# Performance work log

Hardware: AMD Instinct MI355X
Metric: run time of the kernel (lower is better)

## Reference

```python
import jax, jax.numpy as jnp
import numpy as np

B, DIM, HEADS, BLOCKS = 16, 192, 6, 6
H = W = 64
WS, SHIFT, MLP = 8, 4, 4
N = WS * WS
HD = DIM // HEADS
NW = (H // WS) * (W // WS)
SCALE = HD ** -0.5


def _ln(x, g, b, eps=1e-5):
    mu = jnp.mean(x, -1, keepdims=True)
    var = jnp.mean(jnp.square(x - mu), -1, keepdims=True)
    return (x - mu) * jax.lax.rsqrt(var + eps) * g + b


def _win_part(x):  # [B,H,W,C] -> [B*NW, N, C]
    x = x.reshape(B, H // WS, WS, W // WS, WS, DIM)
    return x.transpose(0, 1, 3, 2, 4, 5).reshape(-1, N, DIM)


def _win_rev(w):  # [B*NW, N, C] -> [B,H,W,C]
    x = w.reshape(B, H // WS, W // WS, WS, WS, DIM)
    return x.transpose(0, 1, 3, 2, 4, 5).reshape(B, H, W, DIM)


def _rel_pos_index():
    coords = np.stack(np.meshgrid(np.arange(WS), np.arange(WS), indexing='ij')).reshape(2, -1)
    rel = (coords[:, :, None] - coords[:, None, :]).transpose(1, 2, 0)
    rel[:, :, 0] += WS - 1
    rel[:, :, 1] += WS - 1
    rel[:, :, 0] *= 2 * WS - 1
    return jnp.asarray(rel.sum(-1))  # [N, N] int


def _attn_mask():  # shifted-window attention mask, [NW, N, N]
    img = np.zeros((H, W))
    cnt = 0
    for hs in (slice(0, -WS), slice(-WS, -SHIFT), slice(-SHIFT, None)):
        for ws_ in (slice(0, -WS), slice(-WS, -SHIFT), slice(-SHIFT, None)):
            img[hs, ws_] = cnt
            cnt += 1
    mw = img.reshape(H // WS, WS, W // WS, WS).transpose(0, 2, 1, 3).reshape(-1, N)
    am = mw[:, None, :] - mw[:, :, None]
    return jnp.asarray(np.where(am != 0, -100.0, 0.0).astype(np.float32))


RPI = _rel_pos_index()
MASK = _attn_mask()


def _block(x, shifted, n1g, n1b, qkvw, qkvb, pw, pb, rpb, n2g, n2b, f1w, f1b, f2w, f2b):
    shortcut = x  # [B, H*W, DIM]
    x = _ln(x, n1g, n1b).reshape(B, H, W, DIM)
    if shifted:
        x = jnp.roll(x, (-SHIFT, -SHIFT), (1, 2))
    xw = _win_part(x)  # [B*NW, N, DIM]
    qkv = (xw @ qkvw.T + qkvb).reshape(-1, N, 3, HEADS, HD).transpose(2, 0, 3, 1, 4)
    q, k, v = qkv[0], qkv[1], qkv[2]  # [B*NW, HEADS, N, HD]
    attn = jnp.einsum('bhnd,bhmd->bhnm', q * SCALE, k)
    attn = attn + rpb[RPI].transpose(2, 0, 1)[None]  # relative position bias
    if shifted:
        attn = (attn.reshape(B, NW, HEADS, N, N) + MASK[None, :, None]).reshape(-1, HEADS, N, N)
    attn = jax.nn.softmax(attn, -1)
    xw = jnp.einsum('bhnm,bhmd->bnhd', attn, v).reshape(-1, N, DIM)
    xw = xw @ pw.T + pb
    x = _win_rev(xw)
    if shifted:
        x = jnp.roll(x, (SHIFT, SHIFT), (1, 2))
    x = shortcut + x.reshape(B, H * W, DIM)
    h = _ln(x, n2g, n2b)
    h = jax.nn.gelu(h @ f1w.T + f1b, approximate=False) @ f2w.T + f2b
    return x + h


def _forward(x, en_g, en_b, n1_g, n1_b, qkv_w, qkv_b, proj_w, proj_b, rpb, n2_g, n2_b, fc1_w, fc1_b, fc2_w, fc2_b, fn_g, fn_b, conv_w):
    y = x.reshape(B, DIM, H * W).transpose(0, 2, 1)  # patch embed (patch_size=1)
    y = _ln(y, en_g, en_b)
    for i in range(BLOCKS):
        y = _block(y, i % 2 == 1, n1_g[i], n1_b[i], qkv_w[i], qkv_b[i], proj_w[i], proj_b[i],
                   rpb[i], n2_g[i], n2_b[i], fc1_w[i], fc1_b[i], fc2_w[i], fc2_b[i])
    y = _ln(y, fn_g, fn_b)
    y = y.transpose(0, 2, 1).reshape(B, DIM, H, W)  # patch unembed
    return y + jax.lax.conv_general_dilated(y, conv_w, (1, 1), 'SAME',
                                            dimension_numbers=('NCHW', 'OIHW', 'NCHW'))


def setup_inputs() -> dict:
    key = jax.random.key(0)
    ks = jax.random.split(key, 7)
    s = 0.02
    f32 = jnp.float32
    return {
        'x': jax.random.normal(ks[0], (B, DIM, H, W), f32),
        'en_g': jnp.ones((DIM,), f32), 'en_b': jnp.zeros((DIM,), f32),
        'n1_g': jnp.ones((BLOCKS, DIM), f32), 'n1_b': jnp.zeros((BLOCKS, DIM), f32),
        'qkv_w': s * jax.random.normal(ks[1], (BLOCKS, 3 * DIM, DIM), f32),
        'qkv_b': jnp.zeros((BLOCKS, 3 * DIM), f32),
        'proj_w': s * jax.random.normal(ks[2], (BLOCKS, DIM, DIM), f32),
        'proj_b': jnp.zeros((BLOCKS, DIM), f32),
        'rpb': s * jax.random.normal(ks[3], (BLOCKS, (2 * WS - 1) ** 2, HEADS), f32),
        'n2_g': jnp.ones((BLOCKS, DIM), f32), 'n2_b': jnp.zeros((BLOCKS, DIM), f32),
        'fc1_w': s * jax.random.normal(ks[4], (BLOCKS, MLP * DIM, DIM), f32),
        'fc1_b': jnp.zeros((BLOCKS, MLP * DIM), f32),
        'fc2_w': s * jax.random.normal(ks[5], (BLOCKS, DIM, MLP * DIM), f32),
        'fc2_b': jnp.zeros((BLOCKS, DIM), f32),
        'fn_g': jnp.ones((DIM,), f32), 'fn_b': jnp.zeros((DIM,), f32),
        'conv_w': s * jax.random.normal(ks[6], (DIM, DIM, 3, 3), f32),
    }


def reference(x, en_g, en_b, n1_g, n1_b, qkv_w, qkv_b, proj_w, proj_b, rpb, n2_g, n2_b, fc1_w, fc1_b, fc2_w, fc2_b, fn_g, fn_b, conv_w):
    return _forward(x, en_g, en_b, n1_g, n1_b, qkv_w, qkv_b, proj_w, proj_b, rpb,
                    n2_g, n2_b, fc1_w, fc1_b, fc2_w, fc2_b, fn_g, fn_b, conv_w)
```

## Files before the change

kernel.cpp:

```cpp
#include <hip/hip_runtime.h>
#include <cstdint>
#include <cstddef>

#define BATCH 16
#define DIM 192
#define HEADS 6
#define HD 32
#define TOK 65536
#define QKV_D 576
#define MLP_D 768
#define SCALE 0.17677669529663687f

#define CH 32768

typedef __bf16 bf16x8 __attribute__((ext_vector_type(8)));
typedef float f32x4 __attribute__((ext_vector_type(4)));

__device__ __forceinline__ unsigned short f2bf(float f) {
  union { float f; unsigned u; } c;
  c.f = f;
  return (unsigned short)((c.u + 0x7fffu + ((c.u >> 16) & 1)) >> 16);
}

__device__ __forceinline__ float waveSum(float v) {
#pragma unroll
  for (int off = 32; off; off >>= 1) v += __shfl_xor(v, off, 64);
  return v;
}

__device__ __forceinline__ float rowSum16(float v) {
  v += __shfl_xor(v, 1, 64);
  v += __shfl_xor(v, 2, 64);
  v += __shfl_xor(v, 4, 64);
  v += __shfl_xor(v, 8, 64);
  return v;
}

#define GLD(SRC, DST)                                                     \
  __builtin_amdgcn_global_load_lds(                                       \
      (const __attribute__((address_space(1))) void*)(SRC),               \
      (__attribute__((address_space(3))) void*)(DST), 16, 0, 0)

__global__ __launch_bounds__(64) void zero_k(float* p) { p[threadIdx.x] = 0.f; }

__global__ __launch_bounds__(256) void cvt_k(const float* __restrict__ s,
                                             unsigned short* __restrict__ d,
                                             int n) {
  int i = ((blockIdx.x << 8) + threadIdx.x) << 2;
  if (i < n) {
    float4 v = *(const float4*)(s + i);
    d[i] = f2bf(v.x);
    d[i + 1] = f2bf(v.y);
    d[i + 2] = f2bf(v.z);
    d[i + 3] = f2bf(v.w);
  }
}

__global__ __launch_bounds__(256) void cvt_qkv_k(const float* __restrict__ s,
                                                 unsigned short* __restrict__ d) {
  int i = (blockIdx.x << 8) + threadIdx.x;
  if (i < 663552) {
    int r = (i / 192) % 576;
    float v = s[i];
    if (r < 192) v *= SCALE;
    d[i] = f2bf(v);
  }
}

__global__ __launch_bounds__(256) void scale_qkvb_k(const float* __restrict__ s,
                                                    float* __restrict__ d) {
  int i = (blockIdx.x << 8) + threadIdx.x;
  if (i < 3456) {
    float v = s[i];
    if ((i % 576) < 192) v *= SCALE;
    d[i] = v;
  }
}

__global__ __launch_bounds__(256) void cvt_conv_k(const float* __restrict__ s,
                                                  unsigned short* __restrict__ d) {
  int i = (blockIdx.x << 8) + threadIdx.x;
  if (i < 331776) {
    int o = i / 1728;
    int r = i - o * 1728;
    int tap = r / 192;
    int ci = r - tap * 192;
    d[i] = f2bf(s[o * 1728 + ci * 9 + tap]);
  }
}

__global__ __launch_bounds__(256) void embed_ln_t_k(
    const float* __restrict__ x, const float* __restrict__ g,
    const float* __restrict__ be, float* __restrict__ y) {
  __shared__ float ts[192 * 65];
  const int w = threadIdx.x >> 6, lane = threadIdx.x & 63;
  const int t0 = blockIdx.x << 6;
  const int b = t0 >> 12, tb = t0 & 4095;
  const float* xb = x + (((size_t)b * DIM) << 12) + tb;
#pragma unroll
  for (int j = 0; j < 48; ++j) {
    int ch = w * 48 + j;
    ts[ch * 65 + lane] = xb[((size_t)ch << 12) + lane];
  }
  __syncthreads();
#pragma unroll 4
  for (int idx = 0; idx < 16; ++idx) {
    int tk = (w << 4) + idx;
    float v0 = ts[lane * 65 + tk];
    float v1 = ts[(lane + 64) * 65 + tk];
    float v2 = ts[(lane + 128) * 65 + tk];
    float mu = waveSum(v0 + v1 + v2) * (1.f / 192.f);
    float d0 = v0 - mu, d1 = v1 - mu, d2 = v2 - mu;
    float var = waveSum(d0 * d0 + d1 * d1 + d2 * d2) * (1.f / 192.f);
    float rs = rsqrtf(var + 1e-5f);
    float* yp = y + (size_t)(t0 + tk) * DIM;
    yp[lane] = d0 * rs * g[lane] + be[lane];
    yp[lane + 64] = d1 * rs * g[lane + 64] + be[lane + 64];
    yp[lane + 128] = d2 * rs * g[lane + 128] + be[lane + 128];
  }
}

__global__ __launch_bounds__(256) void ln_final_k(
    float* __restrict__ y, const float* __restrict__ g,
    const float* __restrict__ be, unsigned short* __restrict__ hb) {
  int tok = (blockIdx.x << 2) + (threadIdx.x >> 6);
  int lane = threadIdx.x & 63;
  float* yp = y + (size_t)tok * DIM;
  float v0 = yp[lane], v1 = yp[lane + 64], v2 = yp[lane + 128];
  float mu = waveSum(v0 + v1 + v2) * (1.f / 192.f);
  float d0 = v0 - mu, d1 = v1 - mu, d2 = v2 - mu;
  float var = waveSum(d0 * d0 + d1 * d1 + d2 * d2) * (1.f / 192.f);
  float rs = rsqrtf(var + 1e-5f);
  float r0 = d0 * rs * g[lane] + be[lane];
  float r1 = d1 * rs * g[lane + 64] + be[lane + 64];
  float r2 = d2 * rs * g[lane + 128] + be[lane + 128];
  yp[lane] = r0;
  yp[lane + 64] = r1;
  yp[lane + 128] = r2;
  unsigned short* op = hb + (size_t)tok * DIM;
  op[lane] = f2bf(r0);
  op[lane + 64] = f2bf(r1);
  op[lane + 128] = f2bf(r2);
}

__global__ __launch_bounds__(256) void ln_window_k(
    const float* __restrict__ y, const float* __restrict__ g,
    const float* __restrict__ be, unsigned short* __restrict__ xw,
    int shifted) {
  int m = (blockIdx.x << 2) + (threadIdx.x >> 6);
  int lane = threadIdx.x & 63;
  int widx = m >> 6, n = m & 63;
  int b = widx >> 6, win = widx & 63;
  int hp = ((win >> 3) << 3) + (n >> 3);
  int wp = ((win & 7) << 3) + (n & 7);
  if (shifted) { hp = (hp + 4) & 63; wp = (wp + 4) & 63; }
  int src = (b << 12) + (hp << 6) + wp;
  const float* yp = y + (size_t)src * DIM;
  float v0 = yp[lane], v1 = yp[lane + 64], v2 = yp[lane + 128];
  float mu = waveSum(v0 + v1 + v2) * (1.f / 192.f);
  float d0 = v0 - mu, d1 = v1 - mu, d2 = v2 - mu;
  float var = waveSum(d0 * d0 + d1 * d1 + d2 * d2) * (1.f / 192.f);
  float rs = rsqrtf(var + 1e-5f);
  unsigned short* op = xw + (size_t)m * DIM;
  op[lane] = f2bf(d0 * rs * g[lane] + be[lane]);
  op[lane + 64] = f2bf(d1 * rs * g[lane + 64] + be[lane + 64]);
  op[lane + 128] = f2bf(d2 * rs * g[lane + 128] + be[lane + 128]);
}

__global__ __launch_bounds__(64) void attn_k(
    const unsigned short* __restrict__ qkv, const float* __restrict__ rpb,
    unsigned short* __restrict__ out, int shifted, int widx0) {
  __shared__ unsigned short vt[32 * 72];
  __shared__ unsigned short pl[64 * 72];
  __shared__ float rp[228];
  const int lwidx = blockIdx.x / HEADS;
  const int head = blockIdx.x - lwidx * HEADS;
  const int l = threadIdx.x;
  const int g = l >> 4, li = l & 15;

  for (int i = l; i < 225; i += 64) rp[i] = rpb[i * HEADS + head];

  const unsigned short* base = qkv + (size_t)lwidx * 64 * QKV_D + head * HD;

  bf16x8 qf[4], kf[4];
#pragma unroll
  for (int n = 0; n < 4; ++n)
    qf[n] = *(const bf16x8*)(base + (size_t)(16 * n + li) * QKV_D + g * 8);
#pragma unroll
  for (int i = 0; i < 4; ++i)
    kf[i] = *(const bf16x8*)(base + (size_t)(16 * i + li) * QKV_D + DIM + g * 8);

#pragma unroll
  for (int p = 0; p < 4; ++p) {
    int r = 16 * p + (l >> 2);
    int d0 = (l & 3) << 3;
    bf16x8 v8 = *(const bf16x8*)(base + (size_t)r * QKV_D + 2 * DIM + d0);
#pragma unroll
    for (int e = 0; e < 8; ++e)
      vt[(d0 + e) * 72 + r] = ((const unsigned short*)&v8)[e];
  }

  f32x4 s[4][4] = {};
#pragma unroll
  for (int i = 0; i < 4; ++i)
#pragma unroll
    for (int n = 0; n < 4; ++n)
      s[i][n] = __builtin_amdgcn_mfma_f32_16x16x32_bf16(kf[i], qf[n], s[i][n],
                                                        0, 0, 0);
  __syncthreads();

  const int win = (widx0 + lwidx) & 63;
  const int wh = (win >> 3) << 3, wwp = (win & 7) << 3;
  int rq[4], cq[4], zq[4];
#pragma unroll
  for (int n = 0; n < 4; ++n) {
    int q = 16 * n + li;
    rq[n] = q >> 3;
    cq[n] = q & 7;
    zq[n] = 0;
    if (shifted) {
      int hq = wh + rq[n], wq = wwp + cq[n];
      int zr = hq < 56 ? 0 : (hq < 60 ? 1 : 2);
      int zc = wq < 56 ? 0 : (wq < 60 ? 1 : 2);
      zq[n] = 3 * zr + zc;
    }
  }
#pragma unroll
  for (int i = 0; i < 4; ++i)
#pragma unroll
    for (int j = 0; j < 4; ++j) {
      int m = 16 * i + 4 * g + j;
      int rm = m >> 3, cm = m & 7;
      int zm = 0;
      if (shifted) {
        int hm = wh + rm, wm = wwp + cm;
        int zr = hm < 56 ? 0 : (hm < 60 ? 1 : 2);
        int zc = wm < 56 ? 0 : (wm < 60 ? 1 : 2);
        zm = 3 * zr + zc;
      }
#pragma unroll
      for (int n = 0; n < 4; ++n) {
        float b = rp[(rq[n] - rm + 7) * 15 + (cq[n] - cm + 7)];
        if (shifted && zm != zq[n]) b -= 100.f;
        s[i][n][j] += b;
      }
    }

  float inv[4];
#pragma unroll
  for (int n = 0; n < 4; ++n) {
    float m0 = -1e30f;
#pragma unroll
    for (int i = 0; i < 4; ++i)
#pragma unroll
      for (int j = 0; j < 4; ++j) m0 = fmaxf(m0, s[i][n][j]);
    m0 = fmaxf(m0, __shfl_xor(m0, 16, 64));
    m0 = fmaxf(m0, __shfl_xor(m0, 32, 64));
    float s0 = 0.f;
#pragma unroll
    for (int i = 0; i < 4; ++i)
#pragma unroll
      for (int j = 0; j < 4; ++j) {
        float e = __expf(s[i][n][j] - m0);
        s[i][n][j] = e;
        s0 += e;
      }
    s0 += __shfl_xor(s0, 16, 64);
    s0 += __shfl_xor(s0, 32, 64);
    inv[n] = 1.f / s0;
  }

#pragma unroll
  for (int n = 0; n < 4; ++n) {
    int q = 16 * n + li;
#pragma unroll
    for (int i = 0; i < 4; ++i) {
      unsigned lo = (unsigned)f2bf(s[i][n][0]) | ((unsigned)f2bf(s[i][n][1]) << 16);
      unsigned hi = (unsigned)f2bf(s[i][n][2]) | ((unsigned)f2bf(s[i][n][3]) << 16);
      *(uint2*)&pl[q * 72 + 16 * i + 4 * g] = uint2{lo, hi};
    }
  }
  __syncthreads();

  f32x4 o[2][4] = {};
#pragma unroll
  for (int ks = 0; ks < 2; ++ks) {
    bf16x8 va[2], pb[4];
#pragma unroll
    for (int i2 = 0; i2 < 2; ++i2)
      va[i2] = *(const bf16x8*)&vt[(16 * i2 + li) * 72 + 32 * ks + 8 * g];
#pragma unroll
    for (int n2 = 0; n2 < 4; ++n2)
      pb[n2] = *(const bf16x8*)&pl[(16 * n2 + li) * 72 + 32 * ks + 8 * g];
#pragma unroll
    for (int i2 = 0; i2 < 2; ++i2)
#pragma unroll
      for (int n2 = 0; n2 < 4; ++n2)
        o[i2][n2] = __builtin_amdgcn_mfma_f32_16x16x32_bf16(va[i2], pb[n2],
                                                            o[i2][n2], 0, 0, 0);
  }

  unsigned short* ob = out + (size_t)(lwidx * 64) * DIM + head * HD;
#pragma unroll
  for (int i2 = 0; i2 < 2; ++i2)
#pragma unroll
    for (int n2 = 0; n2 < 4; ++n2) {
      int q = 16 * n2 + li;
      float iv = inv[n2];
      unsigned lo = (unsigned)f2bf(o[i2][n2][0] * iv) |
                    ((unsigned)f2bf(o[i2][n2][1] * iv) << 16);
      unsigned hi = (unsigned)f2bf(o[i2][n2][2] * iv) |
                    ((unsigned)f2bf(o[i2][n2][3] * iv) << 16);
      *(uint2*)(ob + (size_t)q * DIM + 16 * i2 + 4 * g) = uint2{lo, hi};
    }
}

__device__ __forceinline__ void mfma_block256(const unsigned short* As,
                                              const unsigned short* Bs,
                                              f32x4 acc[4][4], int w,
                                              int lane) {
  const int frow = lane & 15;
  const int fk = (lane >> 4) << 3;
#pragma unroll
  for (int kk = 0; kk < 64; kk += 32) {
    int slotk = (kk + fk) >> 3;
    bf16x8 a[4], b[4];
#pragma unroll
    for (int m = 0; m < 4; ++m) {
      int ar = (w << 6) + (m << 4) + frow;
      a[m] = *(const bf16x8*)&As[(ar << 6) + ((slotk ^ (ar & 7)) << 3)];
    }
#pragma unroll
    for (int n = 0; n < 4; ++n) {
      int br = (n << 4) + frow;
      b[n] = *(const bf16x8*)&Bs[(br << 6) + ((slotk ^ (br & 7)) << 3)];
    }
#pragma unroll
    for (int m = 0; m < 4; ++m)
#pragma unroll
      for (int n = 0; n < 4; ++n)
        acc[m][n] =
            __builtin_amdgcn_mfma_f32_16x16x32_bf16(a[m], b[n], acc[m][n], 0,
                                                    0, 0);
  }
}

__device__ __forceinline__ void mfma_block128(const unsigned short* As,
                                              const unsigned short* Bs,
                                              f32x4 acc[2][4], int w,
                                              int lane) {
  const int frow = lane & 15;
  const int fk = (lane >> 4) << 3;
#pragma unroll
  for (int kk = 0; kk < 64; kk += 32) {
    int slotk = (kk + fk) >> 3;
    int ar0 = (w << 5) + frow, ar1 = ar0 + 16;
    bf16x8 a0 = *(const bf16x8*)&As[(ar0 << 6) + ((slotk ^ (ar0 & 7)) << 3)];
    bf16x8 a1 = *(const bf16x8*)&As[(ar1 << 6) + ((slotk ^ (ar1 & 7)) << 3)];
    bf16x8 b[4];
#pragma unroll
    for (int n = 0; n < 4; ++n) {
      int br = (n << 4) + frow;
      b[n] = *(const bf16x8*)&Bs[(br << 6) + ((slotk ^ (br & 7)) << 3)];
    }
#pragma unroll
    for (int n = 0; n < 4; ++n) {
      acc[0][n] = __builtin_amdgcn_mfma_f32_16x16x32_bf16(a0, b[n], acc[0][n], 0, 0, 0);
      acc[1][n] = __builtin_amdgcn_mfma_f32_16x16x32_bf16(a1, b[n], acc[1][n], 0, 0, 0);
    }
  }
}

template <int EPI>
__global__ __launch_bounds__(256) void mgemm_k(
    const unsigned short* __restrict__ A, const unsigned short* __restrict__ W,
    const float* __restrict__ bias, void* __restrict__ Cv, int N, int K) {
  __shared__ unsigned short As[256 * 64];
  __shared__ unsigned short Bs[64 * 64];
  const int tid = threadIdx.x;
  const int w = tid >> 6, lane = tid & 63;
  const int row0 = blockIdx.x << 8;
  const int col0 = blockIdx.y << 6;
  f32x4 acc[4][4] = {};

  for (int k0 = 0; k0 < K; k0 += 64) {
    if (k0) __syncthreads();
#pragma unroll
    for (int r = 0; r < 2; ++r) {
      int q = (r << 8) + tid;
      int brow = q >> 3, cs = q & 7;
      int kg = cs ^ (brow & 7);
      GLD(W + (size_t)(col0 + brow) * K + k0 + (kg << 3),
          Bs + (((r << 8) + (w << 6)) << 3));
    }
#pragma unroll
    for (int r = 0; r < 8; ++r) {
      int q = (r << 8) + tid;
      int arow = q >> 3, cs = q & 7;
      int kg = cs ^ (arow & 7);
      GLD(A + (size_t)(row0 + arow) * K + k0 + (kg << 3),
          As + (((r << 8) + (w << 6)) << 3));
    }
    __syncthreads();
    mfma_block256(As, Bs, acc, w, lane);
  }

  const int erow = (lane >> 4) << 2;
  const int ecol = lane & 15;
#pragma unroll
  for (int mr = 0; mr < 4; ++mr)
#pragma unroll
    for (int nr = 0; nr < 4; ++nr)
#pragma unroll
      for (int j = 0; j < 4; ++j) {
        int row = row0 + (w << 6) + (mr << 4) + erow + j;
        int col = col0 + (nr << 4) + ecol;
        float v = acc[mr][nr][j];
        ((unsigned short*)Cv)[(size_t)row * N + col] = f2bf(v + bias[col]);
      }
}

__global__ __launch_bounds__(256) void wgemm_k(
    const unsigned short* __restrict__ A, const unsigned short* __restrict__ W,
    const float* __restrict__ bias, float* __restrict__ y,
    unsigned short* __restrict__ lnout, const float* __restrict__ g,
    const float* __restrict__ be, int K, int sh2) {
  __shared__ unsigned short As[64 * 64];
  __shared__ unsigned short Bs[192 * 64];
  const int tid = threadIdx.x;
  const int w = tid >> 6, lane = tid & 63;
  const int row0 = blockIdx.x << 6;
  f32x4 acc[12] = {};

  for (int k0 = 0; k0 < K; k0 += 64) {
    if (k0) __syncthreads();
#pragma unroll
    for (int r = 0; r < 6; ++r) {
      int q = (r << 8) + tid;
      int brow = q >> 3, cs = q & 7;
      int kg = cs ^ (brow & 7);
      GLD(W + (size_t)brow * K + k0 + (kg << 3),
          Bs + (((r << 8) + (w << 6)) << 3));
    }
#pragma unroll
    for (int r = 0; r < 2; ++r) {
      int q = (r << 8) + tid;
      int arow = q >> 3, cs = q & 7;
      int kg = cs ^ (arow & 7);
      GLD(A + (size_t)(row0 + arow) * K + k0 + (kg << 3),
          As + (((r << 8) + (w << 6)) << 3));
    }
    __syncthreads();
    const int frow = lane & 15;
    const int fk = (lane >> 4) << 3;
#pragma unroll
    for (int kk = 0; kk < 64; kk += 32) {
      int slotk = (kk + fk) >> 3;
      int ar = (w << 4) + frow;
      bf16x8 a = *(const bf16x8*)&As[(ar << 6) + ((slotk ^ (ar & 7)) << 3)];
      bf16x8 b[12];
#pragma unroll
      for (int n = 0; n < 12; ++n) {
        int br = (n << 4) + frow;
        b[n] = *(const bf16x8*)&Bs[(br << 6) + ((slotk ^ (br & 7)) << 3)];
      }
#pragma unroll
      for (int n = 0; n < 12; ++n)
        acc[n] = __builtin_amdgcn_mfma_f32_16x16x32_bf16(a, b[n], acc[n], 0, 0,
                                                         0);
    }
  }

  const int erow = (lane >> 4) << 2;
  const int ecol = lane & 15;
  float bv[12], gv[12], bev[12];
#pragma unroll
  for (int n = 0; n < 12; ++n) {
    int col = (n << 4) + ecol;
    bv[n] = bias[col];
    gv[n] = g[col];
    bev[n] = be[col];
  }

#pragma unroll
  for (int j = 0; j < 4; ++j) {
    int m = row0 + (w << 4) + erow + j;
    int n64 = m & 63, widx = m >> 6;
    int bl = widx >> 6, win = widx & 63;
    int hp = ((win >> 3) << 3) + (n64 >> 3);
    int wp = ((win & 7) << 3) + (n64 & 7);
    if (sh2) { hp = (hp + 4) & 63; wp = (wp + 4) & 63; }
    int tok = (bl << 12) + (hp << 6) + wp;
    float* yp = y + (size_t)tok * DIM;
    float v[12];
    float s0 = 0.f;
#pragma unroll
    for (int n = 0; n < 12; ++n) {
      v[n] = acc[n][j] + bv[n] + yp[(n << 4) + ecol];
      s0 += v[n];
    }
#pragma unroll
    for (int n = 0; n < 12; ++n) yp[(n << 4) + ecol] = v[n];
    float mu = rowSum16(s0) * (1.f / 192.f);
    float s1 = 0.f;
#pragma unroll
    for (int n = 0; n < 12; ++n) {
      float d = v[n] - mu;
      s1 += d * d;
    }
    float rs = rsqrtf(rowSum16(s1) * (1.f / 192.f) + 1e-5f);
    unsigned short* op = lnout + (size_t)tok * DIM;
#pragma unroll
    for (int n = 0; n < 12; ++n)
      op[(n << 4) + ecol] = f2bf((v[n] - mu) * rs * gv[n] + bev[n]);
  }
}

template <int LAST>
__global__ __launch_bounds__(256) void mlp_k(
    const unsigned short* __restrict__ A, const unsigned short* __restrict__ W1,
    const float* __restrict__ b1, const unsigned short* __restrict__ W2,
    const float* __restrict__ b2, float* __restrict__ y,
    unsigned short* __restrict__ lnout, const float* __restrict__ g,
    const float* __restrict__ be, int sh2) {
  __shared__ unsigned short As[64 * 192];
  __shared__ unsigned short Bsw[192 * 64];
  __shared__ unsigned short hc[64 * 64];
  __shared__ float b1s[768];
  const int tid = threadIdx.x;
  const int w = tid >> 6, lane = tid & 63;
  const int row0 = blockIdx.x << 6;
  const int frow = lane & 15;
  const int fk = (lane >> 4) << 3;
  const int erow = (lane >> 4) << 2;
  const int ecol = lane & 15;

#pragma unroll
  for (int r = 0; r < 6; ++r) {
    int q = (r << 8) + tid;
    int kb = q >> 9, row = (q >> 3) & 63, cs = q & 7;
    int kg = cs ^ (row & 7);
    GLD(A + (size_t)(row0 + row) * 192 + kb * 64 + (kg << 3),
        As + (((r << 8) + (w << 6)) << 3));
  }
  for (int i = tid; i < 768; i += 256) b1s[i] = b1[i];

  f32x4 acc2[12] = {};

  for (int n0 = 0; n0 < 12; ++n0) {
    __syncthreads();
#pragma unroll
    for (int r = 0; r < 6; ++r) {
      int q = (r << 8) + tid;
      int kb = q >> 9, row = (q >> 3) & 63, cs = q & 7;
      int kg = cs ^ (row & 7);
      GLD(W1 + (size_t)(n0 * 64 + row) * 192 + kb * 64 + (kg << 3),
          Bsw + (((r << 8) + (w << 6)) << 3));
    }
    __syncthreads();
    f32x4 acc1[4] = {};
#pragma unroll
    for (int kk = 0; kk < 192; kk += 32) {
      int kb = kk >> 6;
      int slotk = ((kk & 63) + fk) >> 3;
      int ar = (w << 4) + frow;
      bf16x8 a = *(const bf16x8*)&As[(kb << 12) + (ar << 6) +
                                     ((slotk ^ (ar & 7)) << 3)];
#pragma unroll
      for (int n = 0; n < 4; ++n) {
        int br = (n << 4) + frow;
        bf16x8 b = *(const bf16x8*)&Bsw[(kb << 12) + (br << 6) +
                                        ((slotk ^ (br & 7)) << 3)];
        acc1[n] = __builtin_amdgcn_mfma_f32_16x16x32_bf16(a, b, acc1[n], 0, 0, 0);
      }
    }
#pragma unroll
    for (int n = 0; n < 4; ++n)
#pragma unroll
      for (int j = 0; j < 4; ++j) {
        int hr = (w << 4) + erow + j;
        int hcol = (n << 4) + ecol;
        float xg = acc1[n][j] + b1s[n0 * 64 + hcol];
        float hv = 0.5f * xg * (1.f + erff(xg * 0.7071067811865475f));
        hc[(hr << 6) + (((hcol >> 3) ^ (hr & 7)) << 3) + (hcol & 7)] = f2bf(hv);
      }
    __syncthreads();
#pragma unroll
    for (int r = 0; r < 6; ++r) {
      int q = (r << 8) + tid;
      int row = q >> 3, cs = q & 7;
      int kg = cs ^ (row & 7);
      GLD(W2 + (size_t)row * 768 + n0 * 64 + (kg << 3),
          Bsw + (((r << 8) + (w << 6)) << 3));
    }
    __syncthreads();
#pragma unroll
    for (int kk = 0; kk < 64; kk += 32) {
      int slotk = (kk + fk) >> 3;
      int ar = (w << 4) + frow;
      bf16x8 a = *(const bf16x8*)&hc[(ar << 6) + ((slotk ^ (ar & 7)) << 3)];
#pragma unroll
      for (int n = 0; n < 12; ++n) {
        int br = (n << 4) + frow;
        bf16x8 b = *(const bf16x8*)&Bsw[(br << 6) + ((slotk ^ (br & 7)) << 3)];
        acc2[n] = __builtin_amdgcn_mfma_f32_16x16x32_bf16(a, b, acc2[n], 0, 0, 0);
      }
    }
  }

  float bv[12], gv[12], bev[12];
#pragma unroll
  for (int n = 0; n < 12; ++n) {
    int col = (n << 4) + ecol;
    bv[n] = b2[col];
    if (LAST == 0) { gv[n] = g[col]; bev[n] = be[col]; }
  }

#pragma unroll
  for (int j = 0; j < 4; ++j) {
    int tok = row0 + (w << 4) + erow + j;
    float* yp = y + (size_t)tok * DIM;
    float v[12];
    float s0 = 0.f;
#pragma unroll
    for (int n = 0; n < 12; ++n) {
      v[n] = acc2[n][j] + bv[n] + yp[(n << 4) + ecol];
      s0 += v[n];
    }
#pragma unroll
    for (int n = 0; n < 12; ++n) yp[(n << 4) + ecol] = v[n];
    if (LAST == 0) {
      float mu = rowSum16(s0) * (1.f / 192.f);
      float s1 = 0.f;
#pragma unroll
      for (int n = 0; n < 12; ++n) {
        float d = v[n] - mu;
        s1 += d * d;
      }
      float rs = rsqrtf(rowSum16(s1) * (1.f / 192.f) + 1e-5f);
      int hw = tok & 4095;
      int gi = tok >> 12;
      int h = hw >> 6, ww = hw & 63;
      int hs = sh2 ? (h + 60) & 63 : h;
      int ws = sh2 ? (ww + 60) & 63 : ww;
      int win = ((hs >> 3) << 3) | (ws >> 3);
      int n64 = ((hs & 7) << 3) | (ws & 7);
      size_t drow = ((size_t)gi << 12) + (win << 6) + n64;
      unsigned short* op = lnout + drow * DIM;
#pragma unroll
      for (int n = 0; n < 12; ++n)
        op[(n << 4) + ecol] = f2bf((v[n] - mu) * rs * gv[n] + bev[n]);
    }
  }
}

__global__ __launch_bounds__(256) void conv_k(
    const unsigned short* __restrict__ A, const unsigned short* __restrict__ W,
    float* __restrict__ out, const float* __restrict__ Z,
    const unsigned short* __restrict__ zpg) {
  __shared__ unsigned short As[128 * 64];
  __shared__ unsigned short Bs[64 * 64];
  const int tid = threadIdx.x;
  const int w = tid >> 6, lane = tid & 63;
  const int row0 = blockIdx.x << 7;
  const int col0 = blockIdx.y << 6;
  f32x4 acc[2][4] = {};
  bool first = true;

#pragma unroll
  for (int tap = 0; tap < 9; ++tap) {
    const int dh = tap / 3 - 1, dw = tap % 3 - 1;
#pragma unroll
    for (int k0 = 0; k0 < 192; k0 += 64) {
      if (!first) __syncthreads();
      first = false;
#pragma unroll
      for (int r = 0; r < 2; ++r) {
        int q = (r << 8) + tid;
        int brow = q >> 3, cs = q & 7;
        int kg = cs ^ (brow & 7);
        GLD(W + (size_t)(col0 + brow) * 1728 + tap * 192 + k0 + (kg << 3),
            Bs + (((r << 8) + (w << 6)) << 3));
      }
#pragma unroll
      for (int r = 0; r < 4; ++r) {
        int q = (r << 8) + tid;
        int arow = q >> 3, cs = q & 7;
        int kg = cs ^ (arow & 7);
        int m = row0 + arow;
        int hw_ = m & 4095;
        int h = hw_ >> 6, ww = hw_ & 63;
        int ih = h + dh, iw = ww + dw;
        const unsigned short* src =
            ((unsigned)ih < 64u && (unsigned)iw < 64u)
                ? A + (size_t)(m + dh * 64 + dw) * DIM + k0 + (kg << 3)
                : zpg;
        GLD(src, As + (((r << 8) + (w << 6)) << 3));
      }
      __syncthreads();
      mfma_block128(As, Bs, acc, w, lane);
    }
  }

  const int erow = (lane >> 4) << 2;
  const int ecol = lane & 15;
#pragma unroll
  for (int mr = 0; mr < 2; ++mr)
#pragma unroll
    for (int nr = 0; nr < 4; ++nr)
#pragma unroll
      for (int j = 0; j < 4; ++j) {
        int row = row0 + (w << 5) + (mr << 4) + erow + j;
        int col = col0 + (nr << 4) + ecol;
        int b = row >> 12, hw_ = row & 4095;
        out[(((size_t)(b * DIM + col)) << 12) + hw_] =
            acc[mr][nr][j] + Z[(size_t)row * DIM + col];
      }
}

extern "C" void kernel_launch(void* const* d_in, const int* in_sizes, int n_in,
                              void* d_out, int out_size, void* d_ws,
                              size_t ws_size, hipStream_t stream) {
  const float* x = (const float*)d_in[0];
  const float* en_g = (const float*)d_in[1];
  const float* en_b = (const float*)d_in[2];
  const float* n1_g = (const float*)d_in[3];
  const float* n1_b = (const float*)d_in[4];
  const float* qkv_w = (const float*)d_in[5];
  const float* qkv_b = (const float*)d_in[6];
  const float* proj_w = (const float*)d_in[7];
  const float* proj_b = (const float*)d_in[8];
  const float* rpb = (const float*)d_in[9];
  const float* n2_g = (const float*)d_in[10];
  const float* n2_b = (const float*)d_in[11];
  const float* fc1_w = (const float*)d_in[12];
  const float* fc1_b = (const float*)d_in[13];
  const float* fc2_w = (const float*)d_in[14];
  const float* fc2_b = (const float*)d_in[15];
  const float* fn_g = (const float*)d_in[16];
  const float* fn_b = (const float*)d_in[17];
  const float* conv_w = (const float*)d_in[18];
  float* out = (float*)d_out;

  float* y = (float*)d_ws;
  unsigned short* buf1 = (unsigned short*)((char*)d_ws + 50331648);
  unsigned short* buf2u = (unsigned short*)((char*)d_ws + 75497472);
  unsigned short* ln2buf = buf2u;
  unsigned short* wbuf = (unsigned short*)((char*)d_ws + 113246208);
  unsigned short* zpg = (unsigned short*)((char*)d_ws + 119218176);
  float* qkv_bs = (float*)((char*)d_ws + 119218432);

  unsigned short* qkv_wb = wbuf;
  unsigned short* proj_wb = wbuf + 663552;
  unsigned short* fc1_wb = wbuf + 884736;
  unsigned short* fc2_wb = wbuf + 1769472;
  unsigned short* conv_wb = wbuf + 2654208;

  zero_k<<<1, 64, 0, stream>>>((float*)zpg);
  cvt_qkv_k<<<2592, 256, 0, stream>>>(qkv_w, qkv_wb);
  scale_qkvb_k<<<14, 256, 0, stream>>>(qkv_b, qkv_bs);
  cvt_k<<<216, 256, 0, stream>>>(proj_w, proj_wb, 221184);
  cvt_k<<<864, 256, 0, stream>>>(fc1_w, fc1_wb, 884736);
  cvt_k<<<864, 256, 0, stream>>>(fc2_w, fc2_wb, 884736);
  cvt_conv_k<<<1296, 256, 0, stream>>>(conv_w, conv_wb);

  embed_ln_t_k<<<1024, 256, 0, stream>>>(x, en_g, en_b, y);
  ln_window_k<<<16384, 256, 0, stream>>>(y, n1_g, n1_b, buf1, 0);

  for (int i = 0; i < 6; ++i) {
    int sh = i & 1;
    for (int c = 0; c < 2; ++c) {
      unsigned short* b1c = buf1 + (size_t)c * CH * DIM;
      mgemm_k<3><<<dim3(CH / 256, 9), 256, 0, stream>>>(
          b1c, qkv_wb + (size_t)i * QKV_D * DIM, qkv_bs + i * QKV_D, buf2u,
          QKV_D, DIM);
      attn_k<<<(CH / 64) * HEADS, 64, 0, stream>>>(
          buf2u, rpb + i * 225 * HEADS, b1c, sh, c * (CH / 64));
    }
    wgemm_k<<<TOK / 64, 256, 0, stream>>>(
        buf1, proj_wb + (size_t)i * DIM * DIM, proj_b + i * DIM, y, ln2buf,
        n2_g + i * DIM, n2_b + i * DIM, DIM, sh);
    if (i < 5) {
      mlp_k<0><<<TOK / 64, 256, 0, stream>>>(
          ln2buf, fc1_wb + (size_t)i * MLP_D * DIM, fc1_b + i * MLP_D,
          fc2_wb + (size_t)i * DIM * MLP_D, fc2_b + i * DIM, y, buf1,
          n1_g + (i + 1) * DIM, n1_b + (i + 1) * DIM, (i + 1) & 1);
    } else {
      mlp_k<1><<<TOK / 64, 256, 0, stream>>>(
          ln2buf, fc1_wb + (size_t)i * MLP_D * DIM, fc1_b + i * MLP_D,
          fc2_wb + (size_t)i * DIM * MLP_D, fc2_b + i * DIM, y, buf1, fn_g,
          fn_b, 0);
    }
  }

  ln_final_k<<<16384, 256, 0, stream>>>(y, fn_g, fn_b, buf1);
  conv_k<<<dim3(TOK / 128, 3), 256, 0, stream>>>(buf1, conv_wb, out, y, zpg);
}
```

Measured before the change: 1.386 ms.

## Double row tile in proj and MLP kernels, load A fragments directly from global

The projection GEMM and fused MLP kernels now process 128 rows per block (32 per wave, two MFMA row tiles) instead of 64, halving the number of blocks and the number of times weight tiles are staged into LDS. The A operand is no longer staged in shared memory. Each wave reads its bf16x8 fragments straight from global memory, which cuts LDS use and barriers but relies on cache hits for the repeated A reads. Accumulator registers double, which may lower occupancy, and the fc1 stage now reloads A from global on every one of the 12 n0 iterations.

```diff
diff --git a/kernel.cpp b/kernel.cpp
--- a/kernel.cpp
+++ b/kernel.cpp
@@ -425,12 +425,13 @@
     const float* __restrict__ bias, float* __restrict__ y,
     unsigned short* __restrict__ lnout, const float* __restrict__ g,
     const float* __restrict__ be, int K, int sh2) {
-  __shared__ unsigned short As[64 * 64];
   __shared__ unsigned short Bs[192 * 64];
   const int tid = threadIdx.x;
   const int w = tid >> 6, lane = tid & 63;
-  const int row0 = blockIdx.x << 6;
-  f32x4 acc[12] = {};
+  const int row0 = blockIdx.x << 7;
+  const int frow = lane & 15;
+  const int fk = (lane >> 4) << 3;
+  f32x4 acc[2][12] = {};
 
   for (int k0 = 0; k0 < K; k0 += 64) {
     if (k0) __syncthreads();
@@ -442,32 +443,23 @@
       GLD(W + (size_t)brow * K + k0 + (kg << 3),
           Bs + (((r << 8) + (w << 6)) << 3));
     }
-#pragma unroll
-    for (int r = 0; r < 2; ++r) {
-      int q = (r << 8) + tid;
-      int arow = q >> 3, cs = q & 7;
-      int kg = cs ^ (arow & 7);
-      GLD(A + (size_t)(row0 + arow) * K + k0 + (kg << 3),
-          As + (((r << 8) + (w << 6)) << 3));
-    }
     __syncthreads();
-    const int frow = lane & 15;
-    const int fk = (lane >> 4) << 3;
 #pragma unroll
     for (int kk = 0; kk < 64; kk += 32) {
       int slotk = (kk + fk) >> 3;
-      int ar = (w << 4) + frow;
-      bf16x8 a = *(const bf16x8*)&As[(ar << 6) + ((slotk ^ (ar & 7)) << 3)];
-      bf16x8 b[12];
-#pragma unroll
-      for (int n = 0; n < 12; ++n) {
-        int br = (n << 4) + frow;
-        b[n] = *(const bf16x8*)&Bs[(br << 6) + ((slotk ^ (br & 7)) << 3)];
-      }
-#pragma unroll
-      for (int n = 0; n < 12; ++n)
-        acc[n] = __builtin_amdgcn_mfma_f32_16x16x32_bf16(a, b[n], acc[n], 0, 0,
-                                                         0);
+#pragma unroll
+      for (int m = 0; m < 2; ++m) {
+        int ar = row0 + (w << 5) + (m << 4) + frow;
+        bf16x8 a = *(const bf16x8*)(A + (size_t)ar * K + k0 + kk + fk);
+        bf16x8 b;
+#pragma unroll
+        for (int n = 0; n < 12; ++n) {
+          int br = (n << 4) + frow;
+          b = *(const bf16x8*)&Bs[(br << 6) + ((slotk ^ (br & 7)) << 3)];
+          acc[m][n] = __builtin_amdgcn_mfma_f32_16x16x32_bf16(a, b, acc[m][n],
+                                                              0, 0, 0);
+        }
+      }
     }
   }
 
@@ -483,37 +475,39 @@
   }
 
 #pragma unroll
-  for (int j = 0; j < 4; ++j) {
-    int m = row0 + (w << 4) + erow + j;
-    int n64 = m & 63, widx = m >> 6;
-    int bl = widx >> 6, win = widx & 63;
-    int hp = ((win >> 3) << 3) + (n64 >> 3);
-    int wp = ((win & 7) << 3) + (n64 & 7);
-    if (sh2) { hp = (hp + 4) & 63; wp = (wp + 4) & 63; }
-    int tok = (bl << 12) + (hp << 6) + wp;
-    float* yp = y + (size_t)tok * DIM;
-    float v[12];
-    float s0 = 0.f;
-#pragma unroll
-    for (int n = 0; n < 12; ++n) {
-      v[n] = acc[n][j] + bv[n] + yp[(n << 4) + ecol];
-      s0 += v[n];
-    }
-#pragma unroll
-    for (int n = 0; n < 12; ++n) yp[(n << 4) + ecol] = v[n];
-    float mu = rowSum16(s0) * (1.f / 192.f);
-    float s1 = 0.f;
-#pragma unroll
-    for (int n = 0; n < 12; ++n) {
-      float d = v[n] - mu;
-      s1 += d * d;
-    }
-    float rs = rsqrtf(rowSum16(s1) * (1.f / 192.f) + 1e-5f);
-    unsigned short* op = lnout + (size_t)tok * DIM;
-#pragma unroll
-    for (int n = 0; n < 12; ++n)
-      op[(n << 4) + ecol] = f2bf((v[n] - mu) * rs * gv[n] + bev[n]);
-  }
+  for (int mr = 0; mr < 2; ++mr)
+#pragma unroll
+    for (int j = 0; j < 4; ++j) {
+      int m = row0 + (w << 5) + (mr << 4) + erow + j;
+      int n64 = m & 63, widx = m >> 6;
+      int bl = widx >> 6, win = widx & 63;
+      int hp = ((win >> 3) << 3) + (n64 >> 3);
+      int wp = ((win & 7) << 3) + (n64 & 7);
+      if (sh2) { hp = (hp + 4) & 63; wp = (wp + 4) & 63; }
+      int tok = (bl << 12) + (hp << 6) + wp;
+      float* yp = y + (size_t)tok * DIM;
+      float v[12];
+      float s0 = 0.f;
+#pragma unroll
+      for (int n = 0; n < 12; ++n) {
+        v[n] = acc[mr][n][j] + bv[n] + yp[(n << 4) + ecol];
+        s0 += v[n];
+      }
+#pragma unroll
+      for (int n = 0; n < 12; ++n) yp[(n << 4) + ecol] = v[n];
+      float mu = rowSum16(s0) * (1.f / 192.f);
+      float s1 = 0.f;
+#pragma unroll
+      for (int n = 0; n < 12; ++n) {
+        float d = v[n] - mu;
+        s1 += d * d;
+      }
+      float rs = rsqrtf(rowSum16(s1) * (1.f / 192.f) + 1e-5f);
+      unsigned short* op = lnout + (size_t)tok * DIM;
+#pragma unroll
+      for (int n = 0; n < 12; ++n)
+        op[(n << 4) + ecol] = f2bf((v[n] - mu) * rs * gv[n] + bev[n]);
+    }
 }
 
 template <int LAST>
@@ -523,29 +517,20 @@
     const float* __restrict__ b2, float* __restrict__ y,
     unsigned short* __restrict__ lnout, const float* __restrict__ g,
     const float* __restrict__ be, int sh2) {
-  __shared__ unsigned short As[64 * 192];
   __shared__ unsigned short Bsw[192 * 64];
-  __shared__ unsigned short hc[64 * 64];
+  __shared__ unsigned short hc[128 * 64];
   __shared__ float b1s[768];
   const int tid = threadIdx.x;
   const int w = tid >> 6, lane = tid & 63;
-  const int row0 = blockIdx.x << 6;
+  const int row0 = blockIdx.x << 7;
   const int frow = lane & 15;
   const int fk = (lane >> 4) << 3;
   const int erow = (lane >> 4) << 2;
   const int ecol = lane & 15;
 
-#pragma unroll
-  for (int r = 0; r < 6; ++r) {
-    int q = (r << 8) + tid;
-    int kb = q >> 9, row = (q >> 3) & 63, cs = q & 7;
-    int kg = cs ^ (row & 7);
-    GLD(A + (size_t)(row0 + row) * 192 + kb * 64 + (kg << 3),
-        As + (((r << 8) + (w << 6)) << 3));
-  }
   for (int i = tid; i < 768; i += 256) b1s[i] = b1[i];
 
-  f32x4 acc2[12] = {};
+  f32x4 acc2[2][12] = {};
 
   for (int n0 = 0; n0 < 12; ++n0) {
     __syncthreads();
@@ -558,32 +543,38 @@
           Bsw + (((r << 8) + (w << 6)) << 3));
     }
     __syncthreads();
-    f32x4 acc1[4] = {};
+    f32x4 acc1[2][4] = {};
 #pragma unroll
     for (int kk = 0; kk < 192; kk += 32) {
       int kb = kk >> 6;
       int slotk = ((kk & 63) + fk) >> 3;
-      int ar = (w << 4) + frow;
-      bf16x8 a = *(const bf16x8*)&As[(kb << 12) + (ar << 6) +
-                                     ((slotk ^ (ar & 7)) << 3)];
-#pragma unroll
-      for (int n = 0; n < 4; ++n) {
-        int br = (n << 4) + frow;
-        bf16x8 b = *(const bf16x8*)&Bsw[(kb << 12) + (br << 6) +
-                                        ((slotk ^ (br & 7)) << 3)];
-        acc1[n] = __builtin_amdgcn_mfma_f32_16x16x32_bf16(a, b, acc1[n], 0, 0, 0);
-      }
-    }
-#pragma unroll
-    for (int n = 0; n < 4; ++n)
-#pragma unroll
-      for (int j = 0; j < 4; ++j) {
-        int hr = (w << 4) + erow + j;
-        int hcol = (n << 4) + ecol;
-        float xg = acc1[n][j] + b1s[n0 * 64 + hcol];
-        float hv = 0.5f * xg * (1.f + erff(xg * 0.7071067811865475f));
-        hc[(hr << 6) + (((hcol >> 3) ^ (hr & 7)) << 3) + (hcol & 7)] = f2bf(hv);
-      }
+#pragma unroll
+      for (int m = 0; m < 2; ++m) {
+        int ar = row0 + (w << 5) + (m << 4) + frow;
+        bf16x8 a = *(const bf16x8*)(A + (size_t)ar * 192 + kk + fk);
+#pragma unroll
+        for (int n = 0; n < 4; ++n) {
+          int br = (n << 4) + frow;
+          bf16x8 b = *(const bf16x8*)&Bsw[(kb << 12) + (br << 6) +
+                                          ((slotk ^ (br & 7)) << 3)];
+          acc1[m][n] =
+              __builtin_amdgcn_mfma_f32_16x16x32_bf16(a, b, acc1[m][n], 0, 0, 0);
+        }
+      }
+    }
+#pragma unroll
+    for (int m = 0; m < 2; ++m)
+#pragma unroll
+      for (int n = 0; n < 4; ++n)
+#pragma unroll
+        for (int j = 0; j < 4; ++j) {
+          int hr = (w << 5) + (m << 4) + erow + j;
+          int hcol = (n << 4) + ecol;
+          float xg = acc1[m][n][j] + b1s[n0 * 64 + hcol];
+          float hv = 0.5f * xg * (1.f + erff(xg * 0.7071067811865475f));
+          hc[(hr << 6) + (((hcol >> 3) ^ (hr & 7)) << 3) + (hcol & 7)] =
+              f2bf(hv);
+        }
     __syncthreads();
 #pragma unroll
     for (int r = 0; r < 6; ++r) {
@@ -597,13 +588,18 @@
 #pragma unroll
     for (int kk = 0; kk < 64; kk += 32) {
       int slotk = (kk + fk) >> 3;
-      int ar = (w << 4) + frow;
-      bf16x8 a = *(const bf16x8*)&hc[(ar << 6) + ((slotk ^ (ar & 7)) << 3)];
-#pragma unroll
-      for (int n = 0; n < 12; ++n) {
-        int br = (n << 4) + frow;
-        bf16x8 b = *(const bf16x8*)&Bsw[(br << 6) + ((slotk ^ (br & 7)) << 3)];
-        acc2[n] = __builtin_amdgcn_mfma_f32_16x16x32_bf16(a, b, acc2[n], 0, 0, 0);
+#pragma unroll
+      for (int m = 0; m < 2; ++m) {
+        int ar = (w << 5) + (m << 4) + frow;
+        bf16x8 a = *(const bf16x8*)&hc[(ar << 6) + ((slotk ^ (ar & 7)) << 3)];
+#pragma unroll
+        for (int n = 0; n < 12; ++n) {
+          int br = (n << 4) + frow;
+          bf16x8 b =
+              *(const bf16x8*)&Bsw[(br << 6) + ((slotk ^ (br & 7)) << 3)];
+          acc2[m][n] =
+              __builtin_amdgcn_mfma_f32_16x16x32_bf16(a, b, acc2[m][n], 0, 0, 0);
+        }
       }
     }
   }
@@ -617,41 +613,43 @@
   }
 
 #pragma unroll
-  for (int j = 0; j < 4; ++j) {
-    int tok = row0 + (w << 4) + erow + j;
-    float* yp = y + (size_t)tok * DIM;
-    float v[12];
-    float s0 = 0.f;
-#pragma unroll
-    for (int n = 0; n < 12; ++n) {
-      v[n] = acc2[n][j] + bv[n] + yp[(n << 4) + ecol];
-      s0 += v[n];
-    }
-#pragma unroll
-    for (int n = 0; n < 12; ++n) yp[(n << 4) + ecol] = v[n];
-    if (LAST == 0) {
-      float mu = rowSum16(s0) * (1.f / 192.f);
-      float s1 = 0.f;
+  for (int mr = 0; mr < 2; ++mr)
+#pragma unroll
+    for (int j = 0; j < 4; ++j) {
+      int tok = row0 + (w << 5) + (mr << 4) + erow + j;
+      float* yp = y + (size_t)tok * DIM;
+      float v[12];
+      float s0 = 0.f;
 #pragma unroll
       for (int n = 0; n < 12; ++n) {
-        float d = v[n] - mu;
-        s1 += d * d;
-      }
-      float rs = rsqrtf(rowSum16(s1) * (1.f / 192.f) + 1e-5f);
-      int hw = tok & 4095;
-      int gi = tok >> 12;
-      int h = hw >> 6, ww = hw & 63;
-      int hs = sh2 ? (h + 60) & 63 : h;
-      int ws = sh2 ? (ww + 60) & 63 : ww;
-      int win = ((hs >> 3) << 3) | (ws >> 3);
-      int n64 = ((hs & 7) << 3) | (ws & 7);
-      size_t drow = ((size_t)gi << 12) + (win << 6) + n64;
-      unsigned short* op = lnout + drow * DIM;
-#pragma unroll
-      for (int n = 0; n < 12; ++n)
-        op[(n << 4) + ecol] = f2bf((v[n] - mu) * rs * gv[n] + bev[n]);
-    }
-  }
+        v[n] = acc2[mr][n][j] + bv[n] + yp[(n << 4) + ecol];
+        s0 += v[n];
+      }
+#pragma unroll
+      for (int n = 0; n < 12; ++n) yp[(n << 4) + ecol] = v[n];
+      if (LAST == 0) {
+        float mu = rowSum16(s0) * (1.f / 192.f);
+        float s1 = 0.f;
+#pragma unroll
+        for (int n = 0; n < 12; ++n) {
+          float d = v[n] - mu;
+          s1 += d * d;
+        }
+        float rs = rsqrtf(rowSum16(s1) * (1.f / 192.f) + 1e-5f);
+        int hw = tok & 4095;
+        int gi = tok >> 12;
+        int h = hw >> 6, ww = hw & 63;
+        int hs = sh2 ? (h + 60) & 63 : h;
+        int ws = sh2 ? (ww + 60) & 63 : ww;
+        int win = ((hs >> 3) << 3) | (ws >> 3);
+        int n64 = ((hs & 7) << 3) | (ws & 7);
+        size_t drow = ((size_t)gi << 12) + (win << 6) + n64;
+        unsigned short* op = lnout + drow * DIM;
+#pragma unroll
+        for (int n = 0; n < 12; ++n)
+          op[(n << 4) + ecol] = f2bf((v[n] - mu) * rs * gv[n] + bev[n]);
+      }
+    }
 }
 
 __global__ __launch_bounds__(256) void conv_k(
@@ -777,16 +775,16 @@
       attn_k<<<(CH / 64) * HEADS, 64, 0, stream>>>(
           buf2u, rpb + i * 225 * HEADS, b1c, sh, c * (CH / 64));
     }
-    wgemm_k<<<TOK / 64, 256, 0, stream>>>(
+    wgemm_k<<<TOK / 128, 256, 0, stream>>>(
         buf1, proj_wb + (size_t)i * DIM * DIM, proj_b + i * DIM, y, ln2buf,
         n2_g + i * DIM, n2_b + i * DIM, DIM, sh);
     if (i < 5) {
-      mlp_k<0><<<TOK / 64, 256, 0, stream>>>(
+      mlp_k<0><<<TOK / 128, 256, 0, stream>>>(
           ln2buf, fc1_wb + (size_t)i * MLP_D * DIM, fc1_b + i * MLP_D,
           fc2_wb + (size_t)i * DIM * MLP_D, fc2_b + i * DIM, y, buf1,
           n1_g + (i + 1) * DIM, n1_b + (i + 1) * DIM, (i + 1) & 1);
     } else {
-      mlp_k<1><<<TOK / 64, 256, 0, stream>>>(
+      mlp_k<1><<<TOK / 128, 256, 0, stream>>>(
           ln2buf, fc1_wb + (size_t)i * MLP_D * DIM, fc1_b + i * MLP_D,
           fc2_wb + (size_t)i * DIM * MLP_D, fc2_b + i * DIM, y, buf1, fn_g,
           fn_b, 0);
```

Measured after the change: 1.539 ms. 11.0% more time.
